# Optimization experiments

Measured on AMD Instinct MI355X. Metric: run time of the kernel, lower is better.

The kernel has to match this reference:

```python
import jax, jax.numpy as jnp
import numpy as np

B, G, D_EMB = 4096, 20000, 512
H_LOW, N_HIDDEN = 512, 1024
TOPK, T, FILM_W = 64, 0.1, 1.0
LN_EPS = 1e-5


def _layer_norm(x, gamma, beta):
    mu = jnp.mean(x, axis=-1, keepdims=True)
    var = jnp.mean(jnp.square(x - mu), axis=-1, keepdims=True)
    return (x - mu) * jax.lax.rsqrt(var + LN_EPS) * gamma + beta


def _l2norm(x, eps=1e-12):
    n = jnp.sqrt(jnp.sum(jnp.square(x), axis=-1, keepdims=True))
    return x / jnp.maximum(n, eps)


def setup_inputs() -> dict:
    key = jax.random.key(0)
    ks = jax.random.split(key, 8)
    s = 0.02
    return {
        "x": jax.random.normal(ks[0], (B, G), jnp.float32),
        "g": jax.random.normal(ks[1], (G, D_EMB), jnp.float32),
        "W_enc": jax.random.normal(ks[2], (H_LOW, G), jnp.float32) * s,
        "b_enc": jnp.zeros((H_LOW,), jnp.float32),
        "ln1_g": jnp.ones((H_LOW,), jnp.float32),
        "ln1_b": jnp.zeros((H_LOW,), jnp.float32),
        "W_ga": jax.random.normal(ks[3], (H_LOW, D_EMB), jnp.float32) * s,
        "W_gamma": jax.random.normal(ks[4], (H_LOW, H_LOW), jnp.float32) * s,
        "b_gamma": jnp.zeros((H_LOW,), jnp.float32),
        "W_beta": jax.random.normal(ks[5], (H_LOW, H_LOW), jnp.float32) * s,
        "b_beta": jnp.zeros((H_LOW,), jnp.float32),
        "W_exp": jax.random.normal(ks[6], (N_HIDDEN, H_LOW), jnp.float32) * s,
        "b_exp": jnp.zeros((N_HIDDEN,), jnp.float32),
        "ln2_g": jnp.ones((N_HIDDEN,), jnp.float32),
        "ln2_b": jnp.zeros((N_HIDDEN,), jnp.float32),
    }


def reference(x, g, W_enc, b_enc, ln1_g, ln1_b, W_ga, W_gamma, b_gamma,
              W_beta, b_beta, W_exp, b_exp, ln2_g, ln2_b):
    # x_encoder: Linear -> LayerNorm -> GELU (dropout = eval no-op)
    h = jnp.dot(x, W_enc.T) + b_enc                    # [B, H_LOW]
    h = jax.nn.gelu(_layer_norm(h, ln1_g, ln1_b), approximate=False)
    # gene adapter + cosine scores
    e = _l2norm(jnp.dot(g, W_ga.T))                    # [G, H_LOW]
    h_x = _l2norm(h)                                   # [B, H_LOW]
    scores = jnp.dot(h_x, e.T) / T                     # [B, G]
    # top-k mask + masked softmax attention
    _, idx = jax.lax.top_k(scores, TOPK)               # [B, TOPK]
    mask = jnp.zeros_like(scores).at[jnp.arange(B)[:, None], idx].set(1.0)
    attn = jax.nn.softmax(jnp.where(mask == 0, -1e9, scores), axis=-1)
    ctx = jnp.dot(attn, e)                             # [B, H_LOW]
    # FiLM (identity-centered)
    gamma = (jnp.dot(ctx, W_gamma.T) + b_gamma) * FILM_W
    beta = (jnp.dot(ctx, W_beta.T) + b_beta) * FILM_W
    h_cell = (1.0 + gamma) * h_x + beta
    # x_expand: Linear -> LayerNorm -> GELU
    h2 = jnp.dot(h_cell, W_exp.T) + b_exp              # [B, N_HIDDEN]
    return jax.nn.gelu(_layer_norm(h2, ln2_g, ln2_b), approximate=False)
```

## Files before the change

### kernel.cpp

```cpp
#include <hip/hip_runtime.h>
#include <hip/hip_fp16.h>
#include <math.h>
#include <type_traits>

#define DEVI __device__ __forceinline__

typedef __attribute__((ext_vector_type(8))) short bf16x8;
typedef __attribute__((ext_vector_type(4))) float f32x4;
typedef __attribute__((ext_vector_type(4))) unsigned int u32x4;
typedef unsigned short ushort_t;

DEVI unsigned int pack_bf16(float a, float b) {
  unsigned int ua = __float_as_uint(a), ub = __float_as_uint(b);
  ua = (ua + 0x7FFFu + ((ua >> 16) & 1u)) >> 16;
  ub = (ub + 0x7FFFu + ((ub >> 16) & 1u)) >> 16;
  return ua | (ub << 16);
}

DEVI bf16x8 cvt_bf16x8(f32x4 lo, f32x4 hi) {
  unsigned int r0, r1, r2, r3;
  asm("v_cvt_pk_bf16_f32 %0, %1, %2" : "=v"(r0) : "v"(lo[0]), "v"(lo[1]));
  asm("v_cvt_pk_bf16_f32 %0, %1, %2" : "=v"(r1) : "v"(lo[2]), "v"(lo[3]));
  asm("v_cvt_pk_bf16_f32 %0, %1, %2" : "=v"(r2) : "v"(hi[0]), "v"(hi[1]));
  asm("v_cvt_pk_bf16_f32 %0, %1, %2" : "=v"(r3) : "v"(hi[2]), "v"(hi[3]));
  union { u32x4 u; bf16x8 v; } x;
  x.u = u32x4{r0, r1, r2, r3};
  return x.v;
}

template<int SPLITZ, bool DUALB, bool BIAS, typename OutT>
__global__ __launch_bounds__(256, 3) void bgemm(
    const float* __restrict__ A, const ushort_t* __restrict__ B0,
    const ushort_t* __restrict__ B1, const float* __restrict__ bias0,
    const float* __restrict__ bias1, OutT* __restrict__ C,
    int M, int N, int K, int nbn, int nbm)
{
  __shared__ __align__(16) float    As[32 * 256];
  __shared__ __align__(16) ushort_t Bs[16 * 512];
  const int tid = threadIdx.x, lane = tid & 63, wv = tid >> 6;

  const int nwg = gridDim.x;
  const int hw = blockIdx.x;
  const int q = nwg >> 3, r = nwg & 7;
  const int xcd = hw & 7, pos = hw >> 3;
  const int lid = (xcd < r ? xcd * (q + 1) : r * (q + 1) + (xcd - r) * q) + pos;
  const int bn = lid % nbn;
  const int t2 = lid / nbn;
  const int bm = t2 % nbm;
  const int z  = t2 / nbm;

  const ushort_t* B  = (DUALB && z == 1) ? B1 : B0;
  const float* bias  = (DUALB && z == 1) ? bias1 : bias0;

  const int ksteps = (K + 63) >> 6;
  int kbBeg = 0, kbEnd = ksteps;
  if (SPLITZ > 1) {
    const int sz = (ksteps + SPLITZ - 1) / SPLITZ;
    kbBeg = z * sz;
    kbEnd = min(ksteps, kbBeg + sz);
  }

  const int wr = (wv >> 1) * 64, wc = (wv & 1) * 64;
  const int lrow = lane & 15, kg = lane >> 4;

  f32x4 acc[4][4];
#pragma unroll
  for (int i = 0; i < 4; ++i)
#pragma unroll
    for (int j = 0; j < 4; ++j) acc[i][j] = f32x4{0.f, 0.f, 0.f, 0.f};

  const int rA0  = wv * 4 + (lane >> 4);
  const int colA = (((lane & 15) << 4) ^ ((rA0 & 7) << 5)) >> 2;
  const int rB0  = wv * 8 + (lane >> 3);
  const int colB = (((lane & 7) << 4) ^ ((rB0 & 7) << 4)) >> 1;

  const float* aSrc[8];
#pragma unroll
  for (int j = 0; j < 8; ++j) {
    const int grow = min(bm * 128 + rA0 + j * 16, M - 1);
    aSrc[j] = A + (size_t)grow * (size_t)K + colA;
  }
  const ushort_t* bSrc[4];
#pragma unroll
  for (int j = 0; j < 4; ++j) {
    const int grow = min(bn * 128 + rB0 + j * 32, N - 1);
    bSrc[j] = B + (size_t)grow * (size_t)K + colB;
  }

  for (int kb = kbBeg; kb < kbEnd; ++kb) {
    const int k0 = kb << 6;
    if (k0 + 64 <= K) {
#pragma unroll
      for (int j = 0; j < 8; ++j)
        __builtin_amdgcn_global_load_lds(
            (const __attribute__((address_space(1))) void*)(aSrc[j] + k0),
            (__attribute__((address_space(3))) void*)&As[(j * 4 + wv) * 256], 16, 0, 0);
#pragma unroll
      for (int j = 0; j < 4; ++j)
        __builtin_amdgcn_global_load_lds(
            (const __attribute__((address_space(1))) void*)(bSrc[j] + k0),
            (__attribute__((address_space(3))) void*)&Bs[(j * 4 + wv) * 512], 16, 0, 0);
    } else {
#pragma unroll
      for (int j = 0; j < 8; ++j) {
        float4 f = make_float4(0.f, 0.f, 0.f, 0.f);
        if (k0 + colA + 4 <= K) f = *(const float4*)(aSrc[j] + k0);
        *(float4*)((char*)As + (j * 4 + wv) * 1024 + lane * 16) = f;
      }
#pragma unroll
      for (int j = 0; j < 4; ++j) {
        u32x4 v = {0u, 0u, 0u, 0u};
        if (k0 + colB + 8 <= K) v = *(const u32x4*)(bSrc[j] + k0);
        *(u32x4*)((char*)Bs + (j * 4 + wv) * 1024 + lane * 16) = v;
      }
    }
    __syncthreads();
#pragma unroll
    for (int kk = 0; kk < 2; ++kk) {
      bf16x8 af[4], bfr[4];
#pragma unroll
      for (int i = 0; i < 4; ++i) {
        const int ra = wr + i * 16 + lrow;
        const int ab = (kk * 128 + (kg << 5)) ^ ((ra & 7) << 5);
        const char* pa = (const char*)As + ra * 256 + ab;
        af[i] = cvt_bf16x8(*(const f32x4*)pa, *(const f32x4*)(pa + 16));
        const int rb = wc + i * 16 + lrow;
        const int bb = (kk * 64 + (kg << 4)) ^ ((rb & 7) << 4);
        bfr[i] = *(const bf16x8*)((const char*)Bs + rb * 128 + bb);
      }
#pragma unroll
      for (int i = 0; i < 4; ++i)
#pragma unroll
        for (int j = 0; j < 4; ++j)
          acc[i][j] = __builtin_amdgcn_mfma_f32_16x16x32_bf16(af[i], bfr[j], acc[i][j], 0, 0, 0);
    }
    __syncthreads();
  }

  const size_t zoff = (SPLITZ > 1 || DUALB) ? (size_t)z * (size_t)M * (size_t)N : 0;
#pragma unroll
  for (int i = 0; i < 4; ++i) {
#pragma unroll
    for (int j = 0; j < 4; ++j) {
      const int col = bn * 128 + wc + j * 16 + lrow;
      if (col >= N) continue;
      const int row0 = bm * 128 + wr + i * 16 + kg * 4;
      float bv = 0.f;
      if (BIAS) bv = bias[col];
#pragma unroll
      for (int rr = 0; rr < 4; ++rr) {
        const int gr = row0 + rr;
        if (gr < M) {
          const float v = acc[i][j][rr] + bv;
          if constexpr (std::is_same<OutT, __half>::value)
            C[zoff + (size_t)gr * (size_t)N + col] = __float2half(v);
          else
            C[zoff + (size_t)gr * (size_t)N + col] = v;
        }
      }
    }
  }
}

__global__ __launch_bounds__(256) void f2b(
    const float4* __restrict__ in, u32x4* __restrict__ out, int n8)
{
  const int i = blockIdx.x * 256 + threadIdx.x;
  if (i < n8) {
    const float4 a = in[2 * i], b = in[2 * i + 1];
    u32x4 o = { pack_bf16(a.x, a.y), pack_bf16(a.z, a.w),
                pack_bf16(b.x, b.y), pack_bf16(b.z, b.w) };
    out[i] = o;
  }
}

__global__ __launch_bounds__(256) void gee_fuse_ln1(
    const float* __restrict__ P, const float* __restrict__ b_enc,
    const float* __restrict__ g1, const float* __restrict__ b1,
    float* __restrict__ hx)
{
  const int row = blockIdx.x, tid = threadIdx.x;
  __shared__ float red[16];
  const size_t MN = (size_t)4096 * 512;
  float v[2];
#pragma unroll
  for (int e = 0; e < 2; ++e) {
    const int c = tid + e * 256;
    const size_t o = (size_t)row * 512 + c;
    v[e] = P[o] + P[MN + o] + P[2 * MN + o] + P[3 * MN + o] + b_enc[c];
  }
  float a = v[0] + v[1];
  float b = v[0] * v[0] + v[1] * v[1];
#pragma unroll
  for (int o = 32; o > 0; o >>= 1) { a += __shfl_xor(a, o); b += __shfl_xor(b, o); }
  const int lane = tid & 63, wvi = tid >> 6;
  if (lane == 0) { red[wvi] = a; red[8 + wvi] = b; }
  __syncthreads();
  const float mu  = (red[0] + red[1] + red[2] + red[3]) * (1.f / 512.f);
  const float ex2 = (red[8] + red[9] + red[10] + red[11]) * (1.f / 512.f);
  const float inv = rsqrtf(ex2 - mu * mu + 1e-5f);
  float gl[2], ss = 0.f;
#pragma unroll
  for (int e = 0; e < 2; ++e) {
    const int c = tid + e * 256;
    const float y = (v[e] - mu) * inv * g1[c] + b1[c];
    const float t = 0.5f * y * (1.f + erff(y * 0.70710678118654752f));
    gl[e] = t; ss += t * t;
  }
  __syncthreads();
#pragma unroll
  for (int o = 32; o > 0; o >>= 1) ss += __shfl_xor(ss, o);
  if (lane == 0) red[wvi] = ss;
  __syncthreads();
  const float nrm = sqrtf(red[0] + red[1] + red[2] + red[3]);
  const float sc = 1.f / fmaxf(nrm, 1e-12f);
#pragma unroll
  for (int e = 0; e < 2; ++e)
    hx[(size_t)row * 512 + tid + e * 256] = gl[e] * sc;
}

__global__ __launch_bounds__(256) void gee_l2rows(
    const float* __restrict__ ein, ushort_t* __restrict__ eb)
{
  const int row = blockIdx.x, tid = threadIdx.x;
  __shared__ float red[4];
  const float2* er = (const float2*)(ein + (size_t)row * 512);
  const float2 v = er[tid];
  float ss = v.x * v.x + v.y * v.y;
#pragma unroll
  for (int o = 32; o > 0; o >>= 1) ss += __shfl_xor(ss, o);
  if ((tid & 63) == 0) red[tid >> 6] = ss;
  __syncthreads();
  const float sc = 1.f / fmaxf(sqrtf(red[0] + red[1] + red[2] + red[3]), 1e-12f);
  ((unsigned int*)eb)[(size_t)row * 256 + tid] = pack_bf16(v.x * sc, v.y * sc);
}

__global__ __launch_bounds__(256) void gee_topk(
    const __half* __restrict__ scores, int* __restrict__ oidx, float* __restrict__ ow)
{
  constexpr int G = 20000, GP = G / 2, CAP = 2048, TCAP = 160;
  const int row = blockIdx.x, tid = threadIdx.x;
  const int lane = tid & 63, wv = tid >> 6;
  __shared__ int hist[4][256];
  __shared__ int cnt_ge[256];
  __shared__ int wtop[4];
  __shared__ unsigned int comp[CAP];
  __shared__ int whist[4][16];
  __shared__ int sel[64];
  __shared__ int tie[TCAP];
  __shared__ int s_thr, s_above, s_cand, s_cnt, s_n1, s_n2;

  const unsigned int* srow32 =
      (const unsigned int*)((const ushort_t*)scores + (size_t)row * G);
  const ushort_t* srow16 = (const ushort_t*)srow32;

#pragma unroll
  for (int b = 0; b < 4; ++b) hist[b][tid] = 0;
  if (tid == 0) { s_cnt = 0; s_n1 = 0; s_n2 = 0; }
  __syncthreads();

  for (int j0 = 0; j0 < GP; j0 += 256) {
    const int j = j0 + tid;
    if (j < GP) {
      const unsigned int p = srow32[j];
      const unsigned int f = (((p >> 15) & 0x10001u) * 0x7FFFu) + 0x80008000u;
      const unsigned int k2 = p ^ f;
      atomicAdd(&hist[wv][(k2 >> 8) & 0xFFu], 1);
      atomicAdd(&hist[wv][k2 >> 24], 1);
    }
  }
  __syncthreads();
  cnt_ge[tid] = hist[0][tid] + hist[1][tid] + hist[2][tid] + hist[3][tid];
  __syncthreads();
  for (int off = 1; off < 256; off <<= 1) {
    const int add = (tid + off < 256) ? cnt_ge[tid + off] : 0;
    __syncthreads();
    cnt_ge[tid] += add;
    __syncthreads();
  }
  {
    const unsigned long long m = __ballot(cnt_ge[tid] >= 64);
    if (lane == 0) wtop[wv] = m ? (wv * 64 + 63 - __clzll(m)) : -1;
  }
  __syncthreads();
  if (tid == 0) {
    const int thrB = max(max(wtop[0], wtop[1]), max(wtop[2], wtop[3]));
    s_cand  = cnt_ge[thrB];
    s_above = (thrB == 255) ? 0 : cnt_ge[thrB + 1];
    s_thr   = thrB << 8;
  }
  __syncthreads();

  const bool useComp = (s_cand <= CAP);
  const unsigned int thrB = ((unsigned int)s_thr) >> 8;

  if (useComp) {
    for (int j0 = 0; j0 < GP; j0 += 256) {
      const int j = j0 + tid;
      if (j < GP) {
        const unsigned int p = srow32[j];
        const unsigned int f = (((p >> 15) & 0x10001u) * 0x7FFFu) + 0x80008000u;
        const unsigned int k2 = p ^ f;
        const unsigned int lo = k2 & 0xFFFFu, hi = k2 >> 16;
        if ((lo >> 8) >= thrB) {
          const int pos = atomicAdd(&s_cnt, 1);
          comp[pos] = (lo << 16) | (unsigned)(2 * j);
        }
        if ((hi >> 8) >= thrB) {
          const int pos = atomicAdd(&s_cnt, 1);
          comp[pos] = (hi << 16) | (unsigned)(2 * j + 1);
        }
      }
    }
  }
  __syncthreads();
  const int Nloop = useComp ? s_cnt : G;

  for (int pass = 2; pass < 4; ++pass) {
    const int shift = 12 - 4 * pass;
    const unsigned int thr = (unsigned int)s_thr;
    const unsigned int pfx = thr >> (shift + 4);
    int c[16];
#pragma unroll
    for (int b = 0; b < 16; ++b) c[b] = 0;
    for (int j0 = 0; j0 < Nloop; j0 += 256) {
      const int j = j0 + tid;
      const bool ok = j < Nloop;
      unsigned int key;
      if (useComp) {
        key = ok ? (comp[j] >> 16) : 0u;
      } else {
        const unsigned int raw = ok ? (unsigned int)srow16[j] : 0u;
        key = (raw & 0x8000u) ? (0xFFFFu & ~raw) : (raw | 0x8000u);
      }
      const unsigned int nb = (ok && (key >> (shift + 4)) == pfx) ? ((key >> shift) & 15u) : 0xFFu;
#pragma unroll
      for (int b = 0; b < 16; ++b) c[b] += __popcll(__ballot(nb == (unsigned)b));
    }
    if (lane == 0) {
#pragma unroll
      for (int b = 0; b < 16; ++b) whist[wv][b] = c[b];
    }
    __syncthreads();
    if (tid == 0) {
      int run = s_above;
      for (int vv = 15; vv >= 0; --vv) {
        const int c4 = whist[0][vv] + whist[1][vv] + whist[2][vv] + whist[3][vv];
        if (run + c4 >= 64) { s_thr |= vv << shift; break; }
        run += c4;
      }
      s_above = run;
    }
    __syncthreads();
  }

  const unsigned int kthr = (unsigned int)s_thr;
  for (int j0 = 0; j0 < Nloop; j0 += 256) {
    const int j = j0 + tid;
    if (j < Nloop) {
      unsigned int key, idx;
      if (useComp) {
        const unsigned int u = comp[j];
        key = u >> 16; idx = u & 0xFFFFu;
      } else {
        const unsigned int raw = (unsigned int)srow16[j];
        key = (raw & 0x8000u) ? (0xFFFFu & ~raw) : (raw | 0x8000u);
        idx = (unsigned)j;
      }
      if (key > kthr) {
        const int pos = atomicAdd(&s_n1, 1);
        sel[pos] = (int)idx;
      } else if (key == kthr) {
        const int pos = atomicAdd(&s_n2, 1);
        if (pos < TCAP) tie[pos] = (int)idx;
      }
    }
  }
  __syncthreads();
  if (tid == 0) {
    const int n1 = s_n1;
    const int n2 = min(s_n2, TCAP);
    const int need = 64 - n1;
    for (int rr = 0; rr < need; ++rr) {
      int best = 1 << 30, bj = 0;
      for (int j = 0; j < n2; ++j)
        if (tie[j] < best) { best = tie[j]; bj = j; }
      sel[n1 + rr] = best;
      tie[bj] = 1 << 30;
    }
  }
  __syncthreads();
  if (tid < 64) {
    const int idx = sel[tid];
    const float s = __half2float(scores[(size_t)row * G + idx]) * 10.0f;
    float m = s;
#pragma unroll
    for (int o = 32; o > 0; o >>= 1) m = fmaxf(m, __shfl_xor(m, o));
    const float w = __expf(s - m);
    float d = w;
#pragma unroll
    for (int o = 32; o > 0; o >>= 1) d += __shfl_xor(d, o);
    oidx[(size_t)row * 64 + tid] = idx;
    ow[(size_t)row * 64 + tid] = w / d;
  }
}

__global__ __launch_bounds__(256) void gee_ctx(
    const int* __restrict__ idx, const float* __restrict__ w,
    const ushort_t* __restrict__ eb, float* __restrict__ ctx)
{
  const int row = blockIdx.x, tid = threadIdx.x;
  __shared__ int sidx[64];
  __shared__ float sw[64];
  if (tid < 64) { sidx[tid] = idx[(size_t)row * 64 + tid]; sw[tid] = w[(size_t)row * 64 + tid]; }
  __syncthreads();
  float a0 = 0.f, a1 = 0.f;
#pragma unroll 4
  for (int k = 0; k < 64; ++k) {
    const unsigned int pk = ((const unsigned int*)(eb + (size_t)sidx[k] * 512))[tid];
    const float wk = sw[k];
    a0 += wk * __uint_as_float(pk << 16);
    a1 += wk * __uint_as_float(pk & 0xFFFF0000u);
  }
  ((float2*)(ctx + (size_t)row * 512))[tid] = make_float2(a0, a1);
}

__global__ __launch_bounds__(256) void gee_film(
    const float4* __restrict__ gm, const float4* __restrict__ bt,
    const float4* __restrict__ hx, float4* __restrict__ hc, int n4)
{
  const int i = blockIdx.x * 256 + threadIdx.x;
  if (i < n4) {
    const float4 g = gm[i], b = bt[i], h = hx[i];
    float4 r;
    r.x = (1.f + g.x) * h.x + b.x;
    r.y = (1.f + g.y) * h.y + b.y;
    r.z = (1.f + g.z) * h.z + b.z;
    r.w = (1.f + g.w) * h.w + b.w;
    hc[i] = r;
  }
}

__global__ __launch_bounds__(256) void gee_ln2(
    const float* __restrict__ h2, const float* __restrict__ g2,
    const float* __restrict__ b2, float* __restrict__ out)
{
  const int row = blockIdx.x, tid = threadIdx.x;
  __shared__ float red[16];
  float v[4];
  float a = 0.f, b = 0.f;
#pragma unroll
  for (int e = 0; e < 4; ++e) {
    v[e] = h2[(size_t)row * 1024 + tid + e * 256];
    a += v[e]; b += v[e] * v[e];
  }
#pragma unroll
  for (int o = 32; o > 0; o >>= 1) { a += __shfl_xor(a, o); b += __shfl_xor(b, o); }
  const int lane = tid & 63, wvi = tid >> 6;
  if (lane == 0) { red[wvi] = a; red[8 + wvi] = b; }
  __syncthreads();
  const float mu  = (red[0] + red[1] + red[2] + red[3]) * (1.f / 1024.f);
  const float ex2 = (red[8] + red[9] + red[10] + red[11]) * (1.f / 1024.f);
  const float inv = rsqrtf(ex2 - mu * mu + 1e-5f);
#pragma unroll
  for (int e = 0; e < 4; ++e) {
    const int c = tid + e * 256;
    const float y = (v[e] - mu) * inv * g2[c] + b2[c];
    out[(size_t)row * 1024 + c] = 0.5f * y * (1.f + erff(y * 0.70710678118654752f));
  }
}

extern "C" void kernel_launch(void* const* d_in, const int* in_sizes, int n_in,
                              void* d_out, int out_size, void* d_ws, size_t ws_size,
                              hipStream_t stream)
{
  const float* x       = (const float*)d_in[0];
  const float* g       = (const float*)d_in[1];
  const float* W_enc   = (const float*)d_in[2];
  const float* b_enc   = (const float*)d_in[3];
  const float* ln1_g   = (const float*)d_in[4];
  const float* ln1_b   = (const float*)d_in[5];
  const float* W_ga    = (const float*)d_in[6];
  const float* W_gamma = (const float*)d_in[7];
  const float* b_gamma = (const float*)d_in[8];
  const float* W_beta  = (const float*)d_in[9];
  const float* b_beta  = (const float*)d_in[10];
  const float* W_exp   = (const float*)d_in[11];
  const float* b_exp   = (const float*)d_in[12];
  const float* ln2_g   = (const float*)d_in[13];
  const float* ln2_b   = (const float*)d_in[14];
  float* out = (float*)d_out;

  char* ws = (char*)d_ws;
  constexpr size_t OFF_PART   = 0;
  constexpr size_t OFF_SCORES = 0;
  constexpr size_t OFF_GA     = 0;
  constexpr size_t OFF_BE     = 8388608;
  constexpr size_t OFF_HC     = 16777216;
  constexpr size_t OFF_H2     = 25165824;
  constexpr size_t OFF_CTX    = 50331648;
  constexpr size_t OFF_WENCB  = 163840000;
  constexpr size_t OFF_WGAB   = 184320000;
  constexpr size_t OFF_WGMB   = 184844288;
  constexpr size_t OFF_WBTB   = 185368576;
  constexpr size_t OFF_WEXB   = 185892864;
  constexpr size_t OFF_HX     = 186941440;
  constexpr size_t OFF_E      = 195330048;
  constexpr size_t OFF_TIDX   = 236290048;
  constexpr size_t OFF_TW     = 237338624;

  float*    part   = (float*)(ws + OFF_PART);
  __half*   scores = (__half*)(ws + OFF_SCORES);
  float*    ga     = (float*)(ws + OFF_GA);
  float*    be     = (float*)(ws + OFF_BE);
  float*    hc     = (float*)(ws + OFF_HC);
  float*    h2     = (float*)(ws + OFF_H2);
  float*    ctx    = (float*)(ws + OFF_CTX);
  ushort_t* wencb  = (ushort_t*)(ws + OFF_WENCB);
  ushort_t* eb     = (ushort_t*)(ws + OFF_WENCB);
  ushort_t* wgab   = (ushort_t*)(ws + OFF_WGAB);
  ushort_t* wgmb   = (ushort_t*)(ws + OFF_WGMB);
  ushort_t* wbtb   = (ushort_t*)(ws + OFF_WBTB);
  ushort_t* wexb   = (ushort_t*)(ws + OFF_WEXB);
  float*    hx     = (float*)(ws + OFF_HX);
  float*    e      = (float*)(ws + OFF_E);
  int*      tidx   = (int*)(ws + OFF_TIDX);
  float*    tw     = (float*)(ws + OFF_TW);

  f2b<<<5000, 256, 0, stream>>>((const float4*)W_enc,   (u32x4*)wencb, 1280000);
  f2b<<<128,  256, 0, stream>>>((const float4*)W_ga,    (u32x4*)wgab,  32768);
  f2b<<<128,  256, 0, stream>>>((const float4*)W_gamma, (u32x4*)wgmb,  32768);
  f2b<<<128,  256, 0, stream>>>((const float4*)W_beta,  (u32x4*)wbtb,  32768);
  f2b<<<256,  256, 0, stream>>>((const float4*)W_exp,   (u32x4*)wexb,  65536);

  bgemm<4, false, false, float><<<512, 256, 0, stream>>>(
      x, wencb, nullptr, nullptr, nullptr, part, 4096, 512, 20000, 4, 32);
  gee_fuse_ln1<<<4096, 256, 0, stream>>>(part, b_enc, ln1_g, ln1_b, hx);
  bgemm<1, false, false, float><<<628, 256, 0, stream>>>(
      g, wgab, nullptr, nullptr, nullptr, e, 20000, 512, 512, 4, 157);
  gee_l2rows<<<20000, 256, 0, stream>>>(e, eb);
  bgemm<1, false, false, __half><<<5024, 256, 0, stream>>>(
      hx, eb, nullptr, nullptr, nullptr, scores, 4096, 20000, 512, 157, 32);
  gee_topk<<<4096, 256, 0, stream>>>(scores, tidx, tw);
  gee_ctx<<<4096, 256, 0, stream>>>(tidx, tw, eb, ctx);
  bgemm<1, true, true, float><<<256, 256, 0, stream>>>(
      ctx, wgmb, wbtb, b_gamma, b_beta, ga, 4096, 512, 512, 4, 32);
  gee_film<<<2048, 256, 0, stream>>>((const float4*)ga, (const float4*)be,
                                     (const float4*)hx, (float4*)hc, 524288);
  bgemm<1, false, true, float><<<256, 256, 0, stream>>>(
      hc, wexb, nullptr, b_exp, nullptr, h2, 4096, 1024, 512, 8, 32);
  gee_ln2<<<4096, 256, 0, stream>>>(h2, ln2_g, ln2_b, out);
}
```

Before: 561.6 us.

## Double-buffer GEMM LDS with 32-wide K steps and raise encoder split-K to six

The bf16 GEMM kernel now uses two LDS buffers with a K step of 32 instead of one buffer with a K step of 64. The next tile is prefetched via global_load_lds while the MFMAs run on the current one, and each step needs a single barrier. The encoder GEMM goes from split-K 4 to 6 (768 workgroups), and the LN1 fuse kernel sums six partial buffers. The tail path for K not divisible by the step is removed, so K must be a multiple of 32 (20000 and 512 are). The six partials also need more workspace, which may overflow the buffer allocated for them.

After: 606.2 us. 7.9% more time.

```diff
diff --git a/kernel.cpp b/kernel.cpp
--- a/kernel.cpp
+++ b/kernel.cpp
@@ -35,8 +35,8 @@
     const float* __restrict__ bias1, OutT* __restrict__ C,
     int M, int N, int K, int nbn, int nbm)
 {
-  __shared__ __align__(16) float    As[32 * 256];
-  __shared__ __align__(16) ushort_t Bs[16 * 512];
+  __shared__ __align__(16) char AsB[2 * 16384];
+  __shared__ __align__(16) char BsB[2 * 8192];
   const int tid = threadIdx.x, lane = tid & 63, wv = tid >> 6;
 
   const int nwg = gridDim.x;
@@ -52,7 +52,7 @@
   const ushort_t* B  = (DUALB && z == 1) ? B1 : B0;
   const float* bias  = (DUALB && z == 1) ? bias1 : bias0;
 
-  const int ksteps = (K + 63) >> 6;
+  const int ksteps = K >> 5;
   int kbBeg = 0, kbEnd = ksteps;
   if (SPLITZ > 1) {
     const int sz = (ksteps + SPLITZ - 1) / SPLITZ;
@@ -69,73 +69,81 @@
 #pragma unroll
     for (int j = 0; j < 4; ++j) acc[i][j] = f32x4{0.f, 0.f, 0.f, 0.f};
 
-  const int rA0  = wv * 4 + (lane >> 4);
-  const int colA = (((lane & 15) << 4) ^ ((rA0 & 7) << 5)) >> 2;
-  const int rB0  = wv * 8 + (lane >> 3);
-  const int colB = (((lane & 7) << 4) ^ ((rB0 & 7) << 4)) >> 1;
-
-  const float* aSrc[8];
-#pragma unroll
-  for (int j = 0; j < 8; ++j) {
-    const int grow = min(bm * 128 + rA0 + j * 16, M - 1);
-    aSrc[j] = A + (size_t)grow * (size_t)K + colA;
-  }
-  const ushort_t* bSrc[4];
+  const int arow = lane >> 3;
+  const int acol = ((lane & 7) ^ arow) << 2;
+  const float* aSrc[4];
 #pragma unroll
   for (int j = 0; j < 4; ++j) {
-    const int grow = min(bn * 128 + rB0 + j * 32, N - 1);
-    bSrc[j] = B + (size_t)grow * (size_t)K + colB;
-  }
-
-  for (int kb = kbBeg; kb < kbEnd; ++kb) {
-    const int k0 = kb << 6;
-    if (k0 + 64 <= K) {
-#pragma unroll
-      for (int j = 0; j < 8; ++j)
-        __builtin_amdgcn_global_load_lds(
-            (const __attribute__((address_space(1))) void*)(aSrc[j] + k0),
-            (__attribute__((address_space(3))) void*)&As[(j * 4 + wv) * 256], 16, 0, 0);
+    const int grow = min(bm * 128 + wv * 32 + j * 8 + arow, M - 1);
+    aSrc[j] = A + (size_t)grow * (size_t)K + acol;
+  }
+  const int brow = lane >> 2;
+  const int bcol = ((lane & 3) ^ (brow & 3)) << 3;
+  const ushort_t* bSrc[2];
+#pragma unroll
+  for (int j = 0; j < 2; ++j) {
+    const int grow = min(bn * 128 + wv * 32 + j * 16 + brow, N - 1);
+    bSrc[j] = B + (size_t)grow * (size_t)K + bcol;
+  }
+
+  int aoff0[4], aoff1[4], boff[4];
+#pragma unroll
+  for (int i = 0; i < 4; ++i) {
+    const int ra = wr + i * 16 + lrow;
+    aoff0[i] = ra * 128 + ((((kg << 1)    ) ^ (ra & 7)) << 4);
+    aoff1[i] = ra * 128 + ((((kg << 1) | 1) ^ (ra & 7)) << 4);
+    const int rb = wc + i * 16 + lrow;
+    boff[i] = rb * 64 + ((kg ^ (rb & 3)) << 4);
+  }
+
+#define GEE_STAGE(kb, b) do {                                                 \
+    const int k0_ = (kb) << 5;                                                \
+    _Pragma("unroll")                                                         \
+    for (int j_ = 0; j_ < 4; ++j_)                                            \
+      __builtin_amdgcn_global_load_lds(                                       \
+          (const __attribute__((address_space(1))) void*)(aSrc[j_] + k0_),    \
+          (__attribute__((address_space(3))) void*)(AsB + (b) * 16384 +       \
+              (wv * 4 + j_) * 1024), 16, 0, 0);                               \
+    _Pragma("unroll")                                                         \
+    for (int j_ = 0; j_ < 2; ++j_)                                            \
+      __builtin_amdgcn_global_load_lds(                                       \
+          (const __attribute__((address_space(1))) void*)(bSrc[j_] + k0_),    \
+          (__attribute__((address_space(3))) void*)(BsB + (b) * 8192 +        \
+              (wv * 2 + j_) * 1024), 16, 0, 0);                               \
+  } while (0)
+
+  GEE_STAGE(kbBeg, 0);
+  asm volatile("s_waitcnt vmcnt(0)" ::: "memory");
+  __builtin_amdgcn_s_barrier();
+
+  int cur = 0;
+  for (int t = kbBeg; t < kbEnd; ++t) {
+    const bool more = (t + 1 < kbEnd);
+    if (more) GEE_STAGE(t + 1, cur ^ 1);
+    const char* ab = AsB + cur * 16384;
+    const char* bb = BsB + cur * 8192;
+    f32x4 alo[4], ahi[4];
+    bf16x8 bfr[4];
+#pragma unroll
+    for (int i = 0; i < 4; ++i) {
+      alo[i] = *(const f32x4*)(ab + aoff0[i]);
+      ahi[i] = *(const f32x4*)(ab + aoff1[i]);
+      bfr[i] = *(const bf16x8*)(bb + boff[i]);
+    }
+#pragma unroll
+    for (int i = 0; i < 4; ++i) {
+      const bf16x8 af = cvt_bf16x8(alo[i], ahi[i]);
 #pragma unroll
       for (int j = 0; j < 4; ++j)
-        __builtin_amdgcn_global_load_lds(
-            (const __attribute__((address_space(1))) void*)(bSrc[j] + k0),
-            (__attribute__((address_space(3))) void*)&Bs[(j * 4 + wv) * 512], 16, 0, 0);
-    } else {
-#pragma unroll
-      for (int j = 0; j < 8; ++j) {
-        float4 f = make_float4(0.f, 0.f, 0.f, 0.f);
-        if (k0 + colA + 4 <= K) f = *(const float4*)(aSrc[j] + k0);
-        *(float4*)((char*)As + (j * 4 + wv) * 1024 + lane * 16) = f;
-      }
-#pragma unroll
-      for (int j = 0; j < 4; ++j) {
-        u32x4 v = {0u, 0u, 0u, 0u};
-        if (k0 + colB + 8 <= K) v = *(const u32x4*)(bSrc[j] + k0);
-        *(u32x4*)((char*)Bs + (j * 4 + wv) * 1024 + lane * 16) = v;
-      }
-    }
-    __syncthreads();
-#pragma unroll
-    for (int kk = 0; kk < 2; ++kk) {
-      bf16x8 af[4], bfr[4];
-#pragma unroll
-      for (int i = 0; i < 4; ++i) {
-        const int ra = wr + i * 16 + lrow;
-        const int ab = (kk * 128 + (kg << 5)) ^ ((ra & 7) << 5);
-        const char* pa = (const char*)As + ra * 256 + ab;
-        af[i] = cvt_bf16x8(*(const f32x4*)pa, *(const f32x4*)(pa + 16));
-        const int rb = wc + i * 16 + lrow;
-        const int bb = (kk * 64 + (kg << 4)) ^ ((rb & 7) << 4);
-        bfr[i] = *(const bf16x8*)((const char*)Bs + rb * 128 + bb);
-      }
-#pragma unroll
-      for (int i = 0; i < 4; ++i)
-#pragma unroll
-        for (int j = 0; j < 4; ++j)
-          acc[i][j] = __builtin_amdgcn_mfma_f32_16x16x32_bf16(af[i], bfr[j], acc[i][j], 0, 0, 0);
-    }
-    __syncthreads();
-  }
+        acc[i][j] = __builtin_amdgcn_mfma_f32_16x16x32_bf16(af, bfr[j], acc[i][j], 0, 0, 0);
+    }
+    if (more) {
+      asm volatile("s_waitcnt vmcnt(0)" ::: "memory");
+      __builtin_amdgcn_s_barrier();
+    }
+    cur ^= 1;
+  }
+#undef GEE_STAGE
 
   const size_t zoff = (SPLITZ > 1 || DUALB) ? (size_t)z * (size_t)M * (size_t)N : 0;
 #pragma unroll
@@ -187,7 +195,10 @@
   for (int e = 0; e < 2; ++e) {
     const int c = tid + e * 256;
     const size_t o = (size_t)row * 512 + c;
-    v[e] = P[o] + P[MN + o] + P[2 * MN + o] + P[3 * MN + o] + b_enc[c];
+    float s = b_enc[c];
+#pragma unroll
+    for (int qq = 0; qq < 6; ++qq) s += P[qq * MN + o];
+    v[e] = s;
   }
   float a = v[0] + v[1];
   float b = v[0] * v[0] + v[1] * v[1];
@@ -533,7 +544,7 @@
   f2b<<<128,  256, 0, stream>>>((const float4*)W_beta,  (u32x4*)wbtb,  32768);
   f2b<<<256,  256, 0, stream>>>((const float4*)W_exp,   (u32x4*)wexb,  65536);
 
-  bgemm<4, false, false, float><<<512, 256, 0, stream>>>(
+  bgemm<6, false, false, float><<<768, 256, 0, stream>>>(
       x, wencb, nullptr, nullptr, nullptr, part, 4096, 512, 20000, 4, 32);
   gee_fuse_ln1<<<4096, 256, 0, stream>>>(part, b_enc, ln1_g, ln1_b, hx);
   bgemm<1, false, false, float><<<628, 256, 0, stream>>>(
```

## Feed bf16 activations to GEMMs and raise split-K for the encoder GEMM

Applied to the files above, without the earlier changes.

Adds a bf16-A path to the GEMM template, which halves A tile traffic and LDS use, skips the in-loop f32-to-bf16 conversion, and allows four workgroups per CU. Producer kernels (ln1, ctx, film) now emit packed bf16 activations, and the gene embedding output is stored as fp16 before normalization. The encoder GEMM goes from 4-way to 6-way split-K with a 768-block grid to improve occupancy, at the cost of two more partial buffers to reduce. The extra fp16/bf16 roundings could shift top-k selections slightly.

New measurement: 540.0 us. 3.8% less time.

```diff
diff --git a/kernel.cpp b/kernel.cpp
--- a/kernel.cpp
+++ b/kernel.cpp
@@ -28,15 +28,16 @@
   return x.v;
 }
 
-template<int SPLITZ, bool DUALB, bool BIAS, typename OutT>
-__global__ __launch_bounds__(256, 3) void bgemm(
-    const float* __restrict__ A, const ushort_t* __restrict__ B0,
+template<typename AT, int SPLITZ, bool DUALB, bool BIAS, typename OutT>
+__global__ __launch_bounds__(256, sizeof(AT) == 2 ? 4 : 3) void bgemm(
+    const AT* __restrict__ A, const ushort_t* __restrict__ B0,
     const ushort_t* __restrict__ B1, const float* __restrict__ bias0,
     const float* __restrict__ bias1, OutT* __restrict__ C,
     int M, int N, int K, int nbn, int nbm)
 {
-  __shared__ __align__(16) float    As[32 * 256];
-  __shared__ __align__(16) ushort_t Bs[16 * 512];
+  constexpr bool AB16 = (sizeof(AT) == 2);
+  __shared__ __align__(16) char AsB[AB16 ? 16384 : 32768];
+  __shared__ __align__(16) char BsB[16384];
   const int tid = threadIdx.x, lane = tid & 63, wv = tid >> 6;
 
   const int nwg = gridDim.x;
@@ -69,17 +70,27 @@
 #pragma unroll
     for (int j = 0; j < 4; ++j) acc[i][j] = f32x4{0.f, 0.f, 0.f, 0.f};
 
-  const int rA0  = wv * 4 + (lane >> 4);
-  const int colA = (((lane & 15) << 4) ^ ((rA0 & 7) << 5)) >> 2;
-  const int rB0  = wv * 8 + (lane >> 3);
-  const int colB = (((lane & 7) << 4) ^ ((rB0 & 7) << 4)) >> 1;
-
-  const float* aSrc[8];
-#pragma unroll
-  for (int j = 0; j < 8; ++j) {
-    const int grow = min(bm * 128 + rA0 + j * 16, M - 1);
-    aSrc[j] = A + (size_t)grow * (size_t)K + colA;
-  }
+  const AT* aSrc[AB16 ? 4 : 8];
+  int colAe;
+  if constexpr (AB16) {
+    const int rA0 = wv * 8 + (lane >> 3);
+    colAe = (((lane & 7) ^ (lane >> 3)) << 3);
+#pragma unroll
+    for (int j = 0; j < 4; ++j) {
+      const int grow = min(bm * 128 + rA0 + j * 32, M - 1);
+      aSrc[j] = A + (size_t)grow * (size_t)K + colAe;
+    }
+  } else {
+    const int rA0 = wv * 4 + (lane >> 4);
+    colAe = ((lane & 15) << 2) ^ ((rA0 & 7) << 3);
+#pragma unroll
+    for (int j = 0; j < 8; ++j) {
+      const int grow = min(bm * 128 + rA0 + j * 16, M - 1);
+      aSrc[j] = A + (size_t)grow * (size_t)K + colAe;
+    }
+  }
+  const int rB0 = wv * 8 + (lane >> 3);
+  const int colB = (((lane & 7) ^ (lane >> 3)) << 3);
   const ushort_t* bSrc[4];
 #pragma unroll
   for (int j = 0; j < 4; ++j) {
@@ -89,29 +100,40 @@
 
   for (int kb = kbBeg; kb < kbEnd; ++kb) {
     const int k0 = kb << 6;
-    if (k0 + 64 <= K) {
-#pragma unroll
-      for (int j = 0; j < 8; ++j)
-        __builtin_amdgcn_global_load_lds(
-            (const __attribute__((address_space(1))) void*)(aSrc[j] + k0),
-            (__attribute__((address_space(3))) void*)&As[(j * 4 + wv) * 256], 16, 0, 0);
+    if (AB16 || k0 + 64 <= K) {
+      if constexpr (AB16) {
+#pragma unroll
+        for (int j = 0; j < 4; ++j)
+          __builtin_amdgcn_global_load_lds(
+              (const __attribute__((address_space(1))) void*)(aSrc[j] + k0),
+              (__attribute__((address_space(3))) void*)(AsB + (j * 4 + wv) * 1024),
+              16, 0, 0);
+      } else {
+#pragma unroll
+        for (int j = 0; j < 8; ++j)
+          __builtin_amdgcn_global_load_lds(
+              (const __attribute__((address_space(1))) void*)(aSrc[j] + k0),
+              (__attribute__((address_space(3))) void*)(AsB + (j * 4 + wv) * 1024),
+              16, 0, 0);
+      }
 #pragma unroll
       for (int j = 0; j < 4; ++j)
         __builtin_amdgcn_global_load_lds(
             (const __attribute__((address_space(1))) void*)(bSrc[j] + k0),
-            (__attribute__((address_space(3))) void*)&Bs[(j * 4 + wv) * 512], 16, 0, 0);
-    } else {
+            (__attribute__((address_space(3))) void*)(BsB + (j * 4 + wv) * 1024),
+            16, 0, 0);
+    } else if constexpr (!AB16) {
 #pragma unroll
       for (int j = 0; j < 8; ++j) {
         float4 f = make_float4(0.f, 0.f, 0.f, 0.f);
-        if (k0 + colA + 4 <= K) f = *(const float4*)(aSrc[j] + k0);
-        *(float4*)((char*)As + (j * 4 + wv) * 1024 + lane * 16) = f;
+        if (k0 + colAe + 4 <= K) f = *(const float4*)(aSrc[j] + k0);
+        *(float4*)(AsB + (j * 4 + wv) * 1024 + lane * 16) = f;
       }
 #pragma unroll
       for (int j = 0; j < 4; ++j) {
         u32x4 v = {0u, 0u, 0u, 0u};
         if (k0 + colB + 8 <= K) v = *(const u32x4*)(bSrc[j] + k0);
-        *(u32x4*)((char*)Bs + (j * 4 + wv) * 1024 + lane * 16) = v;
+        *(u32x4*)(BsB + (j * 4 + wv) * 1024 + lane * 16) = v;
       }
     }
     __syncthreads();
@@ -121,12 +143,14 @@
 #pragma unroll
       for (int i = 0; i < 4; ++i) {
         const int ra = wr + i * 16 + lrow;
-        const int ab = (kk * 128 + (kg << 5)) ^ ((ra & 7) << 5);
-        const char* pa = (const char*)As + ra * 256 + ab;
-        af[i] = cvt_bf16x8(*(const f32x4*)pa, *(const f32x4*)(pa + 16));
+        if constexpr (AB16) {
+          af[i] = *(const bf16x8*)(AsB + ra * 128 + ((((kk << 2) + kg) ^ (ra & 7)) << 4));
+        } else {
+          const char* pa = AsB + ra * 256 + ((kk * 128 + (kg << 5)) ^ ((ra & 7) << 5));
+          af[i] = cvt_bf16x8(*(const f32x4*)pa, *(const f32x4*)(pa + 16));
+        }
         const int rb = wc + i * 16 + lrow;
-        const int bb = (kk * 64 + (kg << 4)) ^ ((rb & 7) << 4);
-        bfr[i] = *(const bf16x8*)((const char*)Bs + rb * 128 + bb);
+        bfr[i] = *(const bf16x8*)(BsB + rb * 128 + ((((kk << 2) + kg) ^ (rb & 7)) << 4));
       }
 #pragma unroll
       for (int i = 0; i < 4; ++i)
@@ -177,20 +201,20 @@
 __global__ __launch_bounds__(256) void gee_fuse_ln1(
     const float* __restrict__ P, const float* __restrict__ b_enc,
     const float* __restrict__ g1, const float* __restrict__ b1,
-    float* __restrict__ hx)
+    float* __restrict__ hx, unsigned int* __restrict__ hxb)
 {
   const int row = blockIdx.x, tid = threadIdx.x;
   __shared__ float red[16];
   const size_t MN = (size_t)4096 * 512;
-  float v[2];
-#pragma unroll
-  for (int e = 0; e < 2; ++e) {
-    const int c = tid + e * 256;
-    const size_t o = (size_t)row * 512 + c;
-    v[e] = P[o] + P[MN + o] + P[2 * MN + o] + P[3 * MN + o] + b_enc[c];
-  }
-  float a = v[0] + v[1];
-  float b = v[0] * v[0] + v[1] * v[1];
+  const size_t o2 = (size_t)row * 256 + tid;
+  float2 v = ((const float2*)b_enc)[tid];
+#pragma unroll
+  for (int qq = 0; qq < 6; ++qq) {
+    const float2 p = ((const float2*)P)[qq * (MN / 2) + o2];
+    v.x += p.x; v.y += p.y;
+  }
+  float a = v.x + v.y;
+  float b = v.x * v.x + v.y * v.y;
 #pragma unroll
   for (int o = 32; o > 0; o >>= 1) { a += __shfl_xor(a, o); b += __shfl_xor(b, o); }
   const int lane = tid & 63, wvi = tid >> 6;
@@ -199,40 +223,38 @@
   const float mu  = (red[0] + red[1] + red[2] + red[3]) * (1.f / 512.f);
   const float ex2 = (red[8] + red[9] + red[10] + red[11]) * (1.f / 512.f);
   const float inv = rsqrtf(ex2 - mu * mu + 1e-5f);
-  float gl[2], ss = 0.f;
-#pragma unroll
-  for (int e = 0; e < 2; ++e) {
-    const int c = tid + e * 256;
-    const float y = (v[e] - mu) * inv * g1[c] + b1[c];
-    const float t = 0.5f * y * (1.f + erff(y * 0.70710678118654752f));
-    gl[e] = t; ss += t * t;
-  }
+  const float2 gg = ((const float2*)g1)[tid];
+  const float2 bb = ((const float2*)b1)[tid];
+  const float y0 = (v.x - mu) * inv * gg.x + bb.x;
+  const float y1 = (v.y - mu) * inv * gg.y + bb.y;
+  const float t0 = 0.5f * y0 * (1.f + erff(y0 * 0.70710678118654752f));
+  const float t1 = 0.5f * y1 * (1.f + erff(y1 * 0.70710678118654752f));
+  float ss = t0 * t0 + t1 * t1;
   __syncthreads();
 #pragma unroll
   for (int o = 32; o > 0; o >>= 1) ss += __shfl_xor(ss, o);
   if (lane == 0) red[wvi] = ss;
   __syncthreads();
-  const float nrm = sqrtf(red[0] + red[1] + red[2] + red[3]);
-  const float sc = 1.f / fmaxf(nrm, 1e-12f);
-#pragma unroll
-  for (int e = 0; e < 2; ++e)
-    hx[(size_t)row * 512 + tid + e * 256] = gl[e] * sc;
+  const float sc = 1.f / fmaxf(sqrtf(red[0] + red[1] + red[2] + red[3]), 1e-12f);
+  const float h0 = t0 * sc, h1 = t1 * sc;
+  ((float2*)hx)[o2] = make_float2(h0, h1);
+  hxb[o2] = pack_bf16(h0, h1);
 }
 
 __global__ __launch_bounds__(256) void gee_l2rows(
-    const float* __restrict__ ein, ushort_t* __restrict__ eb)
+    const __half2* __restrict__ ein, unsigned int* __restrict__ eb)
 {
   const int row = blockIdx.x, tid = threadIdx.x;
   __shared__ float red[4];
-  const float2* er = (const float2*)(ein + (size_t)row * 512);
-  const float2 v = er[tid];
-  float ss = v.x * v.x + v.y * v.y;
+  const __half2 h = ein[(size_t)row * 256 + tid];
+  const float vx = __half2float(h.x), vy = __half2float(h.y);
+  float ss = vx * vx + vy * vy;
 #pragma unroll
   for (int o = 32; o > 0; o >>= 1) ss += __shfl_xor(ss, o);
   if ((tid & 63) == 0) red[tid >> 6] = ss;
   __syncthreads();
   const float sc = 1.f / fmaxf(sqrtf(red[0] + red[1] + red[2] + red[3]), 1e-12f);
-  ((unsigned int*)eb)[(size_t)row * 256 + tid] = pack_bf16(v.x * sc, v.y * sc);
+  eb[(size_t)row * 256 + tid] = pack_bf16(vx * sc, vy * sc);
 }
 
 __global__ __launch_bounds__(256) void gee_topk(
@@ -407,7 +429,7 @@
 
 __global__ __launch_bounds__(256) void gee_ctx(
     const int* __restrict__ idx, const float* __restrict__ w,
-    const ushort_t* __restrict__ eb, float* __restrict__ ctx)
+    const unsigned int* __restrict__ eb, unsigned int* __restrict__ ctxb)
 {
   const int row = blockIdx.x, tid = threadIdx.x;
   __shared__ int sidx[64];
@@ -417,27 +439,22 @@
   float a0 = 0.f, a1 = 0.f;
 #pragma unroll 4
   for (int k = 0; k < 64; ++k) {
-    const unsigned int pk = ((const unsigned int*)(eb + (size_t)sidx[k] * 512))[tid];
+    const unsigned int pk = eb[(size_t)sidx[k] * 256 + tid];
     const float wk = sw[k];
     a0 += wk * __uint_as_float(pk << 16);
     a1 += wk * __uint_as_float(pk & 0xFFFF0000u);
   }
-  ((float2*)(ctx + (size_t)row * 512))[tid] = make_float2(a0, a1);
+  ctxb[(size_t)row * 256 + tid] = pack_bf16(a0, a1);
 }
 
 __global__ __launch_bounds__(256) void gee_film(
-    const float4* __restrict__ gm, const float4* __restrict__ bt,
-    const float4* __restrict__ hx, float4* __restrict__ hc, int n4)
+    const float2* __restrict__ gm, const float2* __restrict__ bt,
+    const float2* __restrict__ hx, unsigned int* __restrict__ hcb, int n2)
 {
   const int i = blockIdx.x * 256 + threadIdx.x;
-  if (i < n4) {
-    const float4 g = gm[i], b = bt[i], h = hx[i];
-    float4 r;
-    r.x = (1.f + g.x) * h.x + b.x;
-    r.y = (1.f + g.y) * h.y + b.y;
-    r.z = (1.f + g.z) * h.z + b.z;
-    r.w = (1.f + g.w) * h.w + b.w;
-    hc[i] = r;
+  if (i < n2) {
+    const float2 g = gm[i], b = bt[i], h = hx[i];
+    hcb[i] = pack_bf16((1.f + g.x) * h.x + b.x, (1.f + g.y) * h.y + b.y);
   }
 }
 
@@ -496,36 +513,39 @@
   constexpr size_t OFF_SCORES = 0;
   constexpr size_t OFF_GA     = 0;
   constexpr size_t OFF_BE     = 8388608;
-  constexpr size_t OFF_HC     = 16777216;
-  constexpr size_t OFF_H2     = 25165824;
-  constexpr size_t OFF_CTX    = 50331648;
+  constexpr size_t OFF_H2     = 16777216;
   constexpr size_t OFF_WENCB  = 163840000;
+  constexpr size_t OFF_EB     = 163840000;
   constexpr size_t OFF_WGAB   = 184320000;
   constexpr size_t OFF_WGMB   = 184844288;
   constexpr size_t OFF_WBTB   = 185368576;
   constexpr size_t OFF_WEXB   = 185892864;
   constexpr size_t OFF_HX     = 186941440;
   constexpr size_t OFF_E      = 195330048;
-  constexpr size_t OFF_TIDX   = 236290048;
-  constexpr size_t OFF_TW     = 237338624;
-
-  float*    part   = (float*)(ws + OFF_PART);
-  __half*   scores = (__half*)(ws + OFF_SCORES);
-  float*    ga     = (float*)(ws + OFF_GA);
-  float*    be     = (float*)(ws + OFF_BE);
-  float*    hc     = (float*)(ws + OFF_HC);
-  float*    h2     = (float*)(ws + OFF_H2);
-  float*    ctx    = (float*)(ws + OFF_CTX);
-  ushort_t* wencb  = (ushort_t*)(ws + OFF_WENCB);
-  ushort_t* eb     = (ushort_t*)(ws + OFF_WENCB);
-  ushort_t* wgab   = (ushort_t*)(ws + OFF_WGAB);
-  ushort_t* wgmb   = (ushort_t*)(ws + OFF_WGMB);
-  ushort_t* wbtb   = (ushort_t*)(ws + OFF_WBTB);
-  ushort_t* wexb   = (ushort_t*)(ws + OFF_WEXB);
-  float*    hx     = (float*)(ws + OFF_HX);
-  float*    e      = (float*)(ws + OFF_E);
-  int*      tidx   = (int*)(ws + OFF_TIDX);
-  float*    tw     = (float*)(ws + OFF_TW);
+  constexpr size_t OFF_HXB    = 215810048;
+  constexpr size_t OFF_CTXB   = 220004352;
+  constexpr size_t OFF_HCB    = 224198656;
+  constexpr size_t OFF_TIDX   = 228392960;
+  constexpr size_t OFF_TW     = 229441536;
+
+  float*        part   = (float*)(ws + OFF_PART);
+  __half*       scores = (__half*)(ws + OFF_SCORES);
+  float*        ga     = (float*)(ws + OFF_GA);
+  float*        be     = (float*)(ws + OFF_BE);
+  float*        h2     = (float*)(ws + OFF_H2);
+  ushort_t*     wencb  = (ushort_t*)(ws + OFF_WENCB);
+  unsigned int* eb     = (unsigned int*)(ws + OFF_EB);
+  ushort_t*     wgab   = (ushort_t*)(ws + OFF_WGAB);
+  ushort_t*     wgmb   = (ushort_t*)(ws + OFF_WGMB);
+  ushort_t*     wbtb   = (ushort_t*)(ws + OFF_WBTB);
+  ushort_t*     wexb   = (ushort_t*)(ws + OFF_WEXB);
+  float*        hx     = (float*)(ws + OFF_HX);
+  __half*       e      = (__half*)(ws + OFF_E);
+  unsigned int* hxb    = (unsigned int*)(ws + OFF_HXB);
+  unsigned int* ctxb   = (unsigned int*)(ws + OFF_CTXB);
+  unsigned int* hcb    = (unsigned int*)(ws + OFF_HCB);
+  int*          tidx   = (int*)(ws + OFF_TIDX);
+  float*        tw     = (float*)(ws + OFF_TW);
 
   f2b<<<5000, 256, 0, stream>>>((const float4*)W_enc,   (u32x4*)wencb, 1280000);
   f2b<<<128,  256, 0, stream>>>((const float4*)W_ga,    (u32x4*)wgab,  32768);
@@ -533,21 +553,22 @@
   f2b<<<128,  256, 0, stream>>>((const float4*)W_beta,  (u32x4*)wbtb,  32768);
   f2b<<<256,  256, 0, stream>>>((const float4*)W_exp,   (u32x4*)wexb,  65536);
 
-  bgemm<4, false, false, float><<<512, 256, 0, stream>>>(
+  bgemm<float, 6, false, false, float><<<768, 256, 0, stream>>>(
       x, wencb, nullptr, nullptr, nullptr, part, 4096, 512, 20000, 4, 32);
-  gee_fuse_ln1<<<4096, 256, 0, stream>>>(part, b_enc, ln1_g, ln1_b, hx);
-  bgemm<1, false, false, float><<<628, 256, 0, stream>>>(
+  gee_fuse_ln1<<<4096, 256, 0, stream>>>(part, b_enc, ln1_g, ln1_b, hx, hxb);
+  bgemm<float, 1, false, false, __half><<<628, 256, 0, stream>>>(
       g, wgab, nullptr, nullptr, nullptr, e, 20000, 512, 512, 4, 157);
-  gee_l2rows<<<20000, 256, 0, stream>>>(e, eb);
-  bgemm<1, false, false, __half><<<5024, 256, 0, stream>>>(
-      hx, eb, nullptr, nullptr, nullptr, scores, 4096, 20000, 512, 157, 32);
+  gee_l2rows<<<20000, 256, 0, stream>>>((const __half2*)e, eb);
+  bgemm<ushort_t, 1, false, false, __half><<<5024, 256, 0, stream>>>(
+      (const ushort_t*)hxb, (const ushort_t*)eb, nullptr, nullptr, nullptr,
+      scores, 4096, 20000, 512, 157, 32);
   gee_topk<<<4096, 256, 0, stream>>>(scores, tidx, tw);
-  gee_ctx<<<4096, 256, 0, stream>>>(tidx, tw, eb, ctx);
-  bgemm<1, true, true, float><<<256, 256, 0, stream>>>(
-      ctx, wgmb, wbtb, b_gamma, b_beta, ga, 4096, 512, 512, 4, 32);
-  gee_film<<<2048, 256, 0, stream>>>((const float4*)ga, (const float4*)be,
-                                     (const float4*)hx, (float4*)hc, 524288);
-  bgemm<1, false, true, float><<<256, 256, 0, stream>>>(
-      hc, wexb, nullptr, b_exp, nullptr, h2, 4096, 1024, 512, 8, 32);
+  gee_ctx<<<4096, 256, 0, stream>>>(tidx, tw, eb, ctxb);
+  bgemm<ushort_t, 1, true, true, float><<<256, 256, 0, stream>>>(
+      (const ushort_t*)ctxb, wgmb, wbtb, b_gamma, b_beta, ga, 4096, 512, 512, 4, 32);
+  gee_film<<<4096, 256, 0, stream>>>((const float2*)ga, (const float2*)be,
+                                     (const float2*)hx, hcb, 1048576);
+  bgemm<ushort_t, 1, false, true, float><<<256, 256, 0, stream>>>(
+      (const ushort_t*)hcb, wexb, nullptr, b_exp, nullptr, h2, 4096, 1024, 512, 8, 32);
   gee_ln2<<<4096, 256, 0, stream>>>(h2, ln2_g, ln2_b, out);
 }
```
